# Performance work log

Hardware: AMD Instinct MI355X
Metric: run time of the kernel (lower is better)

Reference implementation:

```python
import jax, jax.numpy as jnp
import numpy as np

B, S, DIN, DOUT = 8, 2048, 512, 512

def setup_inputs() -> dict:
    key = jax.random.key(0)
    ks = jax.random.split(key, 9)
    s = 1.0 / np.sqrt(DIN)  # torch Linear default init scale
    return {
        "Q": jax.random.normal(ks[0], (B, S, DIN), jnp.float32),
        "K": jax.random.normal(ks[1], (B, S, DIN), jnp.float32),
        "V": jax.random.normal(ks[2], (B, S, DIN), jnp.float32),
        "Wq": jax.random.uniform(ks[3], (DIN, DOUT), jnp.float32, -s, s),
        "bq": jax.random.uniform(ks[4], (DOUT,), jnp.float32, -s, s),
        "Wk": jax.random.uniform(ks[5], (DIN, DOUT), jnp.float32, -s, s),
        "bk": jax.random.uniform(ks[6], (DOUT,), jnp.float32, -s, s),
        "Wv": jax.random.uniform(ks[7], (DIN, DOUT), jnp.float32, -s, s),
        "bv": jax.random.uniform(ks[8], (DOUT,), jnp.float32, -s, s),
    }

def reference(Q, K, V, Wq, bq, Wk, bk, Wv, bv):
    q = Q @ Wq + bq  # [B,S,D]
    k = K @ Wk + bk
    v = V @ Wv + bv
    # Unscaled attention, exactly as in the torch module
    attn = jnp.einsum('bqd,bkd->bqk', q, k)  # [B,S,S]
    attn_prob = jax.nn.softmax(attn, axis=-1)
    return jnp.einsum('bqk,bkd->bqd', attn_prob, v)
```

## Files before the change

kernel.cpp:

```cpp
#include <hip/hip_runtime.h>
#include <hip/hip_bf16.h>
#include <hip/hip_fp16.h>

#define B_ 8
#define S_ 2048
#define D_ 512

typedef _Float16 f16x8 __attribute__((ext_vector_type(8)));
typedef float f32x4 __attribute__((ext_vector_type(4)));

__device__ __forceinline__ void gload16(const void* g, void* l) {
    __builtin_amdgcn_global_load_lds(
        (const __attribute__((address_space(1))) void*)g,
        (__attribute__((address_space(3))) void*)l, 16, 0, 0);
}

__global__ void wconv_kernel(const float* __restrict__ Wq,
                             const float* __restrict__ Wk,
                             const float* __restrict__ Wv,
                             _Float16* __restrict__ w_ws) {
    int idx = blockIdx.x * 256 + threadIdx.x;
    int which = blockIdx.y;
    const float* W = (which == 0) ? Wq : (which == 1) ? Wk : Wv;
    int n = idx >> 9;
    int k = idx & 511;
    w_ws[(size_t)which * D_ * D_ + (size_t)n * D_ + k] = (_Float16)W[(size_t)k * D_ + n];
}

__launch_bounds__(256)
__global__ void proj_kernel(const float* __restrict__ Q,
                            const float* __restrict__ K,
                            const float* __restrict__ V,
                            const _Float16* __restrict__ w_ws,
                            const float* __restrict__ bq,
                            const float* __restrict__ bk,
                            const float* __restrict__ bv,
                            _Float16* __restrict__ q_ws,
                            _Float16* __restrict__ k_ws,
                            _Float16* __restrict__ v_ws) {
    __shared__ __align__(16) float    As[128 * 32];
    __shared__ __align__(16) _Float16 Bs[128 * 32];

    const int which = blockIdx.z;
    const float* X    = (which == 0) ? Q  : (which == 1) ? K  : V;
    const float* bias = (which == 0) ? bq : (which == 1) ? bk : bv;
    const _Float16* Wt = w_ws + (size_t)which * D_ * D_;

    const int Nb = blockIdx.x * 128;
    const int Mb = blockIdx.y * 128;
    const int t = threadIdx.x;
    const int w = t >> 6;
    const int l = t & 63;
    const int lr = l & 15;
    const int lk = (l >> 4) * 8;
    const int lq = (l >> 4) * 4;

    f32x4 acc[2][8] = {};

    for (int k0 = 0; k0 < D_; k0 += 32) {
        {
            int c = t;
#pragma unroll
            for (int i = 0; i < 4; i++, c += 256) {
                int row = c >> 3, p = c & 7;
                gload16(X + (size_t)(Mb + row) * D_ + k0 + ((p ^ (row & 7)) << 2),
                        As + c * 4);
            }
        }
        {
            int c = t;
#pragma unroll
            for (int i = 0; i < 2; i++, c += 256) {
                int col = c >> 2, p = c & 3;
                gload16(Wt + (size_t)(Nb + col) * D_ + k0 + ((p ^ (col & 3)) << 3),
                        Bs + c * 8);
            }
        }
        __syncthreads();

        f16x8 a[2], b[8];
#pragma unroll
        for (int mi = 0; mi < 2; mi++) {
            int row = w * 32 + mi * 16 + lr;
            int s0 = lk >> 2;
            const float* base = As + row * 32;
            f32x4 a0 = *(const f32x4*)(base + ((s0 ^ (row & 7)) << 2));
            f32x4 a1 = *(const f32x4*)(base + (((s0 + 1) ^ (row & 7)) << 2));
#pragma unroll
            for (int j = 0; j < 4; j++) { a[mi][j] = (_Float16)a0[j]; a[mi][4 + j] = (_Float16)a1[j]; }
        }
#pragma unroll
        for (int ni = 0; ni < 8; ni++) {
            int col = ni * 16 + lr;
            int s = lk >> 3;
            b[ni] = *(const f16x8*)(Bs + col * 32 + ((s ^ (col & 3)) << 3));
        }
#pragma unroll
        for (int mi = 0; mi < 2; mi++)
#pragma unroll
            for (int ni = 0; ni < 8; ni++)
                acc[mi][ni] = __builtin_amdgcn_mfma_f32_16x16x32_f16(a[mi], b[ni], acc[mi][ni], 0, 0, 0);
        __syncthreads();
    }

#pragma unroll
    for (int ni = 0; ni < 8; ni++) {
        int col = Nb + ni * 16 + lr;
        float bn = bias[col];
#pragma unroll
        for (int mi = 0; mi < 2; mi++) {
#pragma unroll
            for (int j = 0; j < 4; j++) {
                int row = Mb + w * 32 + mi * 16 + lq + j;
                float vv = acc[mi][ni][j] + bn;
                if (which == 0) {
                    q_ws[(size_t)row * D_ + col] = (_Float16)vv;
                } else if (which == 1) {
                    k_ws[(size_t)row * D_ + col] = (_Float16)vv;
                } else {
                    int bb = row >> 11, s = row & 2047;
                    v_ws[((size_t)bb * D_ + col) * S_ + s] = (_Float16)vv;
                }
            }
        }
    }
}

__launch_bounds__(512, 4)
__global__ void attn_kernel(const _Float16* __restrict__ q_ws,
                            const _Float16* __restrict__ k_ws,
                            const _Float16* __restrict__ v_ws,
                            float* __restrict__ out) {
    __shared__ __align__(16) float    S_lds[32][260];
    __shared__ __align__(16) _Float16 Q_lds[16384];
    __shared__ float m_lds[32];
    __shared__ float l_lds[32];
    __shared__ float alpha_lds[32];

    const int bid = blockIdx.x;
    const int b  = bid & 7;
    const int qb = (bid >> 3) * 32;

    const int t = threadIdx.x;
    const int w = t >> 6;
    const int l = t & 63;
    const int kc = w;
    const int lr = l & 15;
    const int lk = (l >> 4) * 8;
    const int lq = (l >> 4) * 4;

    const _Float16* qp = q_ws + (size_t)b * S_ * D_;
    const _Float16* kp = k_ws + (size_t)b * S_ * D_;
    const _Float16* vp = v_ws + (size_t)b * D_ * S_;

#pragma unroll
    for (int i = 0; i < 4; i++) {
        int pi = w * 4 + i;
        int ds = pi >> 1, mi = pi & 1;
        gload16(qp + (size_t)(qb + mi * 16 + lr) * D_ + ds * 32 + lk,
                Q_lds + pi * 512 + l * 8);
    }
    if (t < 32) { m_lds[t] = -INFINITY; l_lds[t] = 0.f; }

    f32x4 oacc[2][4] = {};
    __syncthreads();

    for (int kv0 = 0; kv0 < S_; kv0 += 256) {
        f32x4 sacc[2][2] = {};
#pragma unroll 4
        for (int d0 = 0; d0 < D_; d0 += 32) {
            int ds = d0 >> 5;
            f16x8 aq[2], bk2[2];
#pragma unroll
            for (int mi = 0; mi < 2; mi++)
                aq[mi] = *(const f16x8*)(Q_lds + (ds * 2 + mi) * 512 + l * 8);
#pragma unroll
            for (int ni = 0; ni < 2; ni++)
                bk2[ni] = *(const f16x8*)(kp + (size_t)(kv0 + kc * 32 + ni * 16 + lr) * D_ + d0 + lk);
#pragma unroll
            for (int mi = 0; mi < 2; mi++)
#pragma unroll
                for (int ni = 0; ni < 2; ni++)
                    sacc[mi][ni] = __builtin_amdgcn_mfma_f32_16x16x32_f16(aq[mi], bk2[ni], sacc[mi][ni], 0, 0, 0);
        }
#pragma unroll
        for (int mi = 0; mi < 2; mi++)
#pragma unroll
            for (int ni = 0; ni < 2; ni++)
#pragma unroll
                for (int j = 0; j < 4; j++)
                    S_lds[mi * 16 + lq + j][kc * 32 + ni * 16 + lr] = sacc[mi][ni][j];
        __syncthreads();

        {
            const int r = t >> 4;
            const int cs = (t & 15) * 16;
            float sv[16];
#pragma unroll
            for (int c4 = 0; c4 < 4; c4++)
                *(float4*)&sv[c4 * 4] = *(const float4*)&S_lds[r][cs + c4 * 4];
            float mx = sv[0];
#pragma unroll
            for (int c = 1; c < 16; c++) mx = fmaxf(mx, sv[c]);
            mx = fmaxf(mx, __shfl_xor(mx, 1));
            mx = fmaxf(mx, __shfl_xor(mx, 2));
            mx = fmaxf(mx, __shfl_xor(mx, 4));
            mx = fmaxf(mx, __shfl_xor(mx, 8));
            float m_old = m_lds[r];
            float m_new = fmaxf(m_old, mx);
            float ps = 0.f;
            f16x8 p0, p1;
#pragma unroll
            for (int c = 0; c < 8; c++) {
                float p = __expf(sv[c] - m_new);
                ps += p;
                p0[c] = (_Float16)p;
            }
#pragma unroll
            for (int c = 0; c < 8; c++) {
                float p = __expf(sv[c + 8] - m_new);
                ps += p;
                p1[c] = (_Float16)p;
            }
            char* prow = (char*)&S_lds[r][0] + 528;
            *(f16x8*)(prow + cs * 2)      = p0;
            *(f16x8*)(prow + cs * 2 + 16) = p1;
            ps += __shfl_xor(ps, 1);
            ps += __shfl_xor(ps, 2);
            ps += __shfl_xor(ps, 4);
            ps += __shfl_xor(ps, 8);
            if ((t & 15) == 0) {
                float al = __expf(m_old - m_new);
                alpha_lds[r] = al;
                l_lds[r] = l_lds[r] * al + ps;
                m_lds[r] = m_new;
            }
        }
        __syncthreads();

#pragma unroll
        for (int mi = 0; mi < 2; mi++)
#pragma unroll
            for (int j = 0; j < 4; j++) {
                float al = alpha_lds[mi * 16 + lq + j];
#pragma unroll
                for (int ni = 0; ni < 4; ni++) oacc[mi][ni][j] *= al;
            }

#pragma unroll 2
        for (int ks = 0; ks < 8; ks++) {
            f16x8 pa[2], vb[4];
#pragma unroll
            for (int mi = 0; mi < 2; mi++)
                pa[mi] = *(const f16x8*)((const char*)&S_lds[mi * 16 + lr][0] + 528 + (ks * 32 + lk) * 2);
#pragma unroll
            for (int ni = 0; ni < 4; ni++)
                vb[ni] = *(const f16x8*)(vp + (size_t)(kc * 64 + ni * 16 + lr) * S_ + kv0 + ks * 32 + lk);
#pragma unroll
            for (int mi = 0; mi < 2; mi++)
#pragma unroll
                for (int ni = 0; ni < 4; ni++)
                    oacc[mi][ni] = __builtin_amdgcn_mfma_f32_16x16x32_f16(pa[mi], vb[ni], oacc[mi][ni], 0, 0, 0);
        }
        __syncthreads();
    }

#pragma unroll
    for (int mi = 0; mi < 2; mi++)
#pragma unroll
        for (int j = 0; j < 4; j++) {
            int row = mi * 16 + lq + j;
            float rl = 1.f / l_lds[row];
#pragma unroll
            for (int ni = 0; ni < 4; ni++) {
                int col = kc * 64 + ni * 16 + lr;
                out[((size_t)b * S_ + qb + row) * D_ + col] = oacc[mi][ni][j] * rl;
            }
        }
}

extern "C" void kernel_launch(void* const* d_in, const int* in_sizes, int n_in,
                              void* d_out, int out_size, void* d_ws, size_t ws_size,
                              hipStream_t stream) {
    const float* Q  = (const float*)d_in[0];
    const float* K  = (const float*)d_in[1];
    const float* V  = (const float*)d_in[2];
    const float* Wq = (const float*)d_in[3];
    const float* bq = (const float*)d_in[4];
    const float* Wk = (const float*)d_in[5];
    const float* bk = (const float*)d_in[6];
    const float* Wv = (const float*)d_in[7];
    const float* bv = (const float*)d_in[8];
    float* out = (float*)d_out;

    char* ws = (char*)d_ws;
    _Float16* w_ws = (_Float16*)ws;
    _Float16* q_ws = (_Float16*)(ws + 3ull * 512 * 512 * 2);
    _Float16* k_ws = q_ws + 8ull * 2048 * 512;
    _Float16* v_ws = k_ws + 8ull * 2048 * 512;

    wconv_kernel<<<dim3(1024, 3), 256, 0, stream>>>(Wq, Wk, Wv, w_ws);
    proj_kernel<<<dim3(4, 128, 3), 256, 0, stream>>>(Q, K, V, w_ws, bq, bk, bv, q_ws, k_ws, v_ws);
    attn_kernel<<<dim3(512), 512, 0, stream>>>(q_ws, k_ws, v_ws, out);
}
```

Before: 449.4 us.

## Pre-convert inputs to fp16, double-buffer projection, software-pipeline attention loads

Adds a separate kernel that converts Q/K/V activations to fp16 before projection. The projection GEMM now uses fp16 LDS tiles with double buffering and an XCD-aware block remap. The attention kernel drops Q staging in LDS in favour of direct register loads, prefetches K and V fragments ahead of the MFMAs, moves P into its own LDS array, and removes a barrier. The goal is to hide global load latency and shrink LDS traffic, at the cost of an extra fp32-to-fp16 pass over the inputs, more registers and more workspace.

```diff
diff --git a/kernel.cpp b/kernel.cpp
--- a/kernel.cpp
+++ b/kernel.cpp
@@ -7,6 +7,7 @@
 #define D_ 512
 
 typedef _Float16 f16x8 __attribute__((ext_vector_type(8)));
+typedef _Float16 f16x4 __attribute__((ext_vector_type(4)));
 typedef float f32x4 __attribute__((ext_vector_type(4)));
 
 __device__ __forceinline__ void gload16(const void* g, void* l) {
@@ -27,10 +28,28 @@
     w_ws[(size_t)which * D_ * D_ + (size_t)n * D_ + k] = (_Float16)W[(size_t)k * D_ + n];
 }
 
-__launch_bounds__(256)
-__global__ void proj_kernel(const float* __restrict__ Q,
-                            const float* __restrict__ K,
-                            const float* __restrict__ V,
+__global__ void xconv_kernel(const float* __restrict__ Q,
+                             const float* __restrict__ K,
+                             const float* __restrict__ V,
+                             _Float16* __restrict__ x16) {
+    int which = blockIdx.y;
+    const float* X = (which == 0) ? Q : (which == 1) ? K : V;
+    _Float16* dst = x16 + (size_t)which * (16384ull * 512);
+    size_t i0 = ((size_t)blockIdx.x * 256 + threadIdx.x) * 4;
+    const size_t step = 2048ull * 256 * 4;
+#pragma unroll
+    for (int it = 0; it < 4; it++) {
+        size_t i = i0 + (size_t)it * step;
+        float4 v = *(const float4*)(X + i);
+        f16x4 h;
+        h[0] = (_Float16)v.x; h[1] = (_Float16)v.y;
+        h[2] = (_Float16)v.z; h[3] = (_Float16)v.w;
+        *(f16x4*)(dst + i) = h;
+    }
+}
+
+__launch_bounds__(256, 4)
+__global__ void proj_kernel(const _Float16* __restrict__ x16,
                             const _Float16* __restrict__ w_ws,
                             const float* __restrict__ bq,
                             const float* __restrict__ bk,
@@ -38,16 +57,20 @@
                             _Float16* __restrict__ q_ws,
                             _Float16* __restrict__ k_ws,
                             _Float16* __restrict__ v_ws) {
-    __shared__ __align__(16) float    As[128 * 32];
-    __shared__ __align__(16) _Float16 Bs[128 * 32];
+    __shared__ __align__(16) _Float16 As[2][128 * 32];
+    __shared__ __align__(16) _Float16 Bs[2][128 * 32];
 
     const int which = blockIdx.z;
-    const float* X    = (which == 0) ? Q  : (which == 1) ? K  : V;
+    const _Float16* X = x16 + (size_t)which * (16384ull * 512);
     const float* bias = (which == 0) ? bq : (which == 1) ? bk : bv;
     const _Float16* Wt = w_ws + (size_t)which * D_ * D_;
 
-    const int Nb = blockIdx.x * 128;
-    const int Mb = blockIdx.y * 128;
+    const int linear = blockIdx.y * 4 + blockIdx.x;
+    const int xcd = linear & 7;
+    const int i = linear >> 3;
+    const int Mb = (xcd * 16 + (i >> 2)) * 128;
+    const int Nb = (i & 3) * 128;
+
     const int t = threadIdx.x;
     const int w = t >> 6;
     const int l = t & 63;
@@ -55,45 +78,43 @@
     const int lk = (l >> 4) * 8;
     const int lq = (l >> 4) * 4;
 
+#define PROJ_STAGE(buf, k0_)                                                   \
+    do {                                                                       \
+        int c = t;                                                             \
+        _Pragma("unroll")                                                      \
+        for (int r_ = 0; r_ < 2; r_++, c += 256) {                             \
+            int row = c >> 2, p = c & 3;                                       \
+            gload16(X + (size_t)(Mb + row) * D_ + (k0_) + ((p ^ (row & 3)) << 3), \
+                    &As[buf][c * 8]);                                          \
+        }                                                                      \
+        c = t;                                                                 \
+        _Pragma("unroll")                                                      \
+        for (int r_ = 0; r_ < 2; r_++, c += 256) {                             \
+            int col = c >> 2, p = c & 3;                                       \
+            gload16(Wt + (size_t)(Nb + col) * D_ + (k0_) + ((p ^ (col & 3)) << 3), \
+                    &Bs[buf][c * 8]);                                          \
+        }                                                                      \
+    } while (0)
+
     f32x4 acc[2][8] = {};
-
+    PROJ_STAGE(0, 0);
+    __syncthreads();
+
+    int cur = 0;
     for (int k0 = 0; k0 < D_; k0 += 32) {
-        {
-            int c = t;
-#pragma unroll
-            for (int i = 0; i < 4; i++, c += 256) {
-                int row = c >> 3, p = c & 7;
-                gload16(X + (size_t)(Mb + row) * D_ + k0 + ((p ^ (row & 7)) << 2),
-                        As + c * 4);
-            }
-        }
-        {
-            int c = t;
-#pragma unroll
-            for (int i = 0; i < 2; i++, c += 256) {
-                int col = c >> 2, p = c & 3;
-                gload16(Wt + (size_t)(Nb + col) * D_ + k0 + ((p ^ (col & 3)) << 3),
-                        Bs + c * 8);
-            }
-        }
-        __syncthreads();
-
+        if (k0 + 32 < D_) PROJ_STAGE(cur ^ 1, k0 + 32);
+
+        const int s = lk >> 3;
         f16x8 a[2], b[8];
 #pragma unroll
         for (int mi = 0; mi < 2; mi++) {
             int row = w * 32 + mi * 16 + lr;
-            int s0 = lk >> 2;
-            const float* base = As + row * 32;
-            f32x4 a0 = *(const f32x4*)(base + ((s0 ^ (row & 7)) << 2));
-            f32x4 a1 = *(const f32x4*)(base + (((s0 + 1) ^ (row & 7)) << 2));
-#pragma unroll
-            for (int j = 0; j < 4; j++) { a[mi][j] = (_Float16)a0[j]; a[mi][4 + j] = (_Float16)a1[j]; }
+            a[mi] = *(const f16x8*)&As[cur][row * 32 + ((s ^ (row & 3)) << 3)];
         }
 #pragma unroll
         for (int ni = 0; ni < 8; ni++) {
             int col = ni * 16 + lr;
-            int s = lk >> 3;
-            b[ni] = *(const f16x8*)(Bs + col * 32 + ((s ^ (col & 3)) << 3));
+            b[ni] = *(const f16x8*)&Bs[cur][col * 32 + ((s ^ (col & 3)) << 3)];
         }
 #pragma unroll
         for (int mi = 0; mi < 2; mi++)
@@ -101,6 +122,7 @@
             for (int ni = 0; ni < 8; ni++)
                 acc[mi][ni] = __builtin_amdgcn_mfma_f32_16x16x32_f16(a[mi], b[ni], acc[mi][ni], 0, 0, 0);
         __syncthreads();
+        cur ^= 1;
     }
 
 #pragma unroll
@@ -118,8 +140,8 @@
                 } else if (which == 1) {
                     k_ws[(size_t)row * D_ + col] = (_Float16)vv;
                 } else {
-                    int bb = row >> 11, s = row & 2047;
-                    v_ws[((size_t)bb * D_ + col) * S_ + s] = (_Float16)vv;
+                    int bb = row >> 11, s2 = row & 2047;
+                    v_ws[((size_t)bb * D_ + col) * S_ + s2] = (_Float16)vv;
                 }
             }
         }
@@ -132,7 +154,7 @@
                             const _Float16* __restrict__ v_ws,
                             float* __restrict__ out) {
     __shared__ __align__(16) float    S_lds[32][260];
-    __shared__ __align__(16) _Float16 Q_lds[16384];
+    __shared__ __align__(16) _Float16 P_lds[32][272];
     __shared__ float m_lds[32];
     __shared__ float l_lds[32];
     __shared__ float alpha_lds[32];
@@ -153,35 +175,60 @@
     const _Float16* kp = k_ws + (size_t)b * S_ * D_;
     const _Float16* vp = v_ws + (size_t)b * D_ * S_;
 
-#pragma unroll
-    for (int i = 0; i < 4; i++) {
-        int pi = w * 4 + i;
-        int ds = pi >> 1, mi = pi & 1;
-        gload16(qp + (size_t)(qb + mi * 16 + lr) * D_ + ds * 32 + lk,
-                Q_lds + pi * 512 + l * 8);
-    }
+    const _Float16* qrow0 = qp + (size_t)(qb + 0  + lr) * D_ + lk;
+    const _Float16* qrow1 = qp + (size_t)(qb + 16 + lr) * D_ + lk;
+
     if (t < 32) { m_lds[t] = -INFINITY; l_lds[t] = 0.f; }
 
     f32x4 oacc[2][4] = {};
     __syncthreads();
 
+#define QK_LOAD(QB, KB, g)                                                     \
+    do {                                                                       \
+        _Pragma("unroll")                                                      \
+        for (int st = 0; st < 2; st++) {                                       \
+            const int ds = (g) * 2 + st;                                       \
+            QB[st][0] = *(const f16x8*)(qrow0 + ds * 32);                      \
+            QB[st][1] = *(const f16x8*)(qrow1 + ds * 32);                      \
+            _Pragma("unroll")                                                  \
+            for (int ni = 0; ni < 2; ni++)                                     \
+                KB[st][ni] = *(const f16x8*)(krow + (size_t)(ni * 16 + lr) * D_ + ds * 32 + lk); \
+        }                                                                      \
+    } while (0)
+
+#define QK_MFMA(QB, KB)                                                        \
+    do {                                                                       \
+        _Pragma("unroll")                                                      \
+        for (int st = 0; st < 2; st++)                                         \
+            _Pragma("unroll")                                                  \
+            for (int mi = 0; mi < 2; mi++)                                     \
+                _Pragma("unroll")                                              \
+                for (int ni = 0; ni < 2; ni++)                                 \
+                    sacc[mi][ni] = __builtin_amdgcn_mfma_f32_16x16x32_f16(     \
+                        QB[st][mi], KB[st][ni], sacc[mi][ni], 0, 0, 0);        \
+    } while (0)
+
+#define PV_LOADV(VB, ks)                                                       \
+    do {                                                                       \
+        _Pragma("unroll")                                                      \
+        for (int ni = 0; ni < 4; ni++)                                         \
+            VB[ni] = *(const f16x8*)(vrow + (size_t)(ni * 16 + lr) * S_ + (ks) * 32 + lk); \
+    } while (0)
+
     for (int kv0 = 0; kv0 < S_; kv0 += 256) {
         f32x4 sacc[2][2] = {};
-#pragma unroll 4
-        for (int d0 = 0; d0 < D_; d0 += 32) {
-            int ds = d0 >> 5;
-            f16x8 aq[2], bk2[2];
-#pragma unroll
-            for (int mi = 0; mi < 2; mi++)
-                aq[mi] = *(const f16x8*)(Q_lds + (ds * 2 + mi) * 512 + l * 8);
-#pragma unroll
-            for (int ni = 0; ni < 2; ni++)
-                bk2[ni] = *(const f16x8*)(kp + (size_t)(kv0 + kc * 32 + ni * 16 + lr) * D_ + d0 + lk);
-#pragma unroll
-            for (int mi = 0; mi < 2; mi++)
-#pragma unroll
-                for (int ni = 0; ni < 2; ni++)
-                    sacc[mi][ni] = __builtin_amdgcn_mfma_f32_16x16x32_f16(aq[mi], bk2[ni], sacc[mi][ni], 0, 0, 0);
+        const _Float16* krow = kp + (size_t)(kv0 + kc * 32) * D_;
+        {
+            f16x8 qA[2][2], kA[2][2], qB[2][2], kB[2][2];
+            QK_LOAD(qA, kA, 0);
+            QK_LOAD(qB, kB, 1);
+#pragma unroll
+            for (int g = 0; g < 8; g += 2) {
+                QK_MFMA(qA, kA);
+                if (g + 2 < 8) QK_LOAD(qA, kA, g + 2);
+                QK_MFMA(qB, kB);
+                if (g + 3 < 8) QK_LOAD(qB, kB, g + 3);
+            }
         }
 #pragma unroll
         for (int mi = 0; mi < 2; mi++)
@@ -222,9 +269,8 @@
                 ps += p;
                 p1[c] = (_Float16)p;
             }
-            char* prow = (char*)&S_lds[r][0] + 528;
-            *(f16x8*)(prow + cs * 2)      = p0;
-            *(f16x8*)(prow + cs * 2 + 16) = p1;
+            *(f16x8*)&P_lds[r][cs]     = p0;
+            *(f16x8*)&P_lds[r][cs + 8] = p1;
             ps += __shfl_xor(ps, 1);
             ps += __shfl_xor(ps, 2);
             ps += __shfl_xor(ps, 4);
@@ -247,22 +293,34 @@
                 for (int ni = 0; ni < 4; ni++) oacc[mi][ni][j] *= al;
             }
 
-#pragma unroll 2
-        for (int ks = 0; ks < 8; ks++) {
-            f16x8 pa[2], vb[4];
-#pragma unroll
-            for (int mi = 0; mi < 2; mi++)
-                pa[mi] = *(const f16x8*)((const char*)&S_lds[mi * 16 + lr][0] + 528 + (ks * 32 + lk) * 2);
-#pragma unroll
-            for (int ni = 0; ni < 4; ni++)
-                vb[ni] = *(const f16x8*)(vp + (size_t)(kc * 64 + ni * 16 + lr) * S_ + kv0 + ks * 32 + lk);
-#pragma unroll
-            for (int mi = 0; mi < 2; mi++)
-#pragma unroll
-                for (int ni = 0; ni < 4; ni++)
-                    oacc[mi][ni] = __builtin_amdgcn_mfma_f32_16x16x32_f16(pa[mi], vb[ni], oacc[mi][ni], 0, 0, 0);
-        }
-        __syncthreads();
+        {
+            const _Float16* vrow = vp + (size_t)(kc * 64) * S_ + kv0;
+            f16x8 vA[4], vB[4];
+            PV_LOADV(vA, 0);
+            PV_LOADV(vB, 1);
+#pragma unroll
+            for (int ks = 0; ks < 8; ks += 2) {
+                f16x8 pa[2];
+#pragma unroll
+                for (int mi = 0; mi < 2; mi++)
+                    pa[mi] = *(const f16x8*)&P_lds[mi * 16 + lr][ks * 32 + lk];
+#pragma unroll
+                for (int mi = 0; mi < 2; mi++)
+#pragma unroll
+                    for (int ni = 0; ni < 4; ni++)
+                        oacc[mi][ni] = __builtin_amdgcn_mfma_f32_16x16x32_f16(pa[mi], vA[ni], oacc[mi][ni], 0, 0, 0);
+                if (ks + 2 < 8) PV_LOADV(vA, ks + 2);
+#pragma unroll
+                for (int mi = 0; mi < 2; mi++)
+                    pa[mi] = *(const f16x8*)&P_lds[mi * 16 + lr][(ks + 1) * 32 + lk];
+#pragma unroll
+                for (int mi = 0; mi < 2; mi++)
+#pragma unroll
+                    for (int ni = 0; ni < 4; ni++)
+                        oacc[mi][ni] = __builtin_amdgcn_mfma_f32_16x16x32_f16(pa[mi], vB[ni], oacc[mi][ni], 0, 0, 0);
+                if (ks + 3 < 8) PV_LOADV(vB, ks + 3);
+            }
+        }
     }
 
 #pragma unroll
@@ -295,11 +353,13 @@
 
     char* ws = (char*)d_ws;
     _Float16* w_ws = (_Float16*)ws;
-    _Float16* q_ws = (_Float16*)(ws + 3ull * 512 * 512 * 2);
+    _Float16* x16  = (_Float16*)(ws + 3ull * 512 * 512 * 2);
+    _Float16* q_ws = x16 + 3ull * 16384 * 512;
     _Float16* k_ws = q_ws + 8ull * 2048 * 512;
     _Float16* v_ws = k_ws + 8ull * 2048 * 512;
 
     wconv_kernel<<<dim3(1024, 3), 256, 0, stream>>>(Wq, Wk, Wv, w_ws);
-    proj_kernel<<<dim3(4, 128, 3), 256, 0, stream>>>(Q, K, V, w_ws, bq, bk, bv, q_ws, k_ws, v_ws);
+    xconv_kernel<<<dim3(2048, 3), 256, 0, stream>>>(Q, K, V, x16);
+    proj_kernel<<<dim3(4, 128, 3), 256, 0, stream>>>(x16, w_ws, bq, bk, bv, q_ws, k_ws, v_ws);
     attn_kernel<<<dim3(512), 512, 0, stream>>>(q_ws, k_ws, v_ws, out);
 }
```

Measured after the change: 530.9 us. +18.1%, slower.
